# Kernel tuning notes

Hardware: AMD Instinct MI355X
Metric: run time of the kernel (lower is better)

Reference implementation:

```python
import jax, jax.numpy as jnp
import numpy as np

N = 50000      # nodes
E = 800000     # edges
D = 128        # in = out features (required by Euler residual update)
GRID_SIZE = 5
K = 3          # spline order
GRID_LO, GRID_HI = -1.0, 1.0
EPSILON = 0.001
NUM_BASES = GRID_SIZE + K  # 8


def make_grid(in_features):
    # extended uniform grid: [in, grid_size + 2k + 1]
    h = (GRID_HI - GRID_LO) / GRID_SIZE
    g = jnp.arange(-K, GRID_SIZE + K + 1, dtype=jnp.float32) * h + GRID_LO
    return jnp.broadcast_to(g, (in_features, g.shape[0]))


def b_splines(x, grid):
    # x: [N, in]; grid: [in, g+2k+1] -> bases: [N, in, g+k] (Cox-de Boor)
    xe = x[..., None]
    bases = ((xe >= grid[:, :-1]) & (xe < grid[:, 1:])).astype(x.dtype)
    for j in range(1, K + 1):
        left = (xe - grid[:, : -(j + 1)]) / (grid[:, j:-1] - grid[:, : -(j + 1)])
        right = (grid[:, j + 1:] - xe) / (grid[:, j + 1:] - grid[:, 1:-j])
        bases = left * bases[..., :-1] + right * bases[..., 1:]
    return bases


def kan_transform(x, base_w, spline_w, grid):
    # efficient-KAN layer (scale_and_bias=False): silu base branch + spline branch
    base = jax.nn.silu(x) @ base_w.T                    # [N, out]
    sb = b_splines(x, grid)                             # [N, in, g+k]
    spl = jnp.einsum('nib,oib->no', sb, spline_w)       # [N, out]
    return base + spl


def gcn_norm_coeffs(edge_index, n):
    # A_hat symmetric normalization: deg includes self-loop (+1)
    src, dst = edge_index[0], edge_index[1]
    deg = jnp.zeros((n,), jnp.float32).at[dst].add(1.0) + 1.0
    dis = jax.lax.rsqrt(deg)
    return dis[src] * dis[dst]


def setup_inputs() -> dict:
    key = jax.random.key(0)
    ks = jax.random.split(key, 6)
    x = jax.random.uniform(ks[0], (N, D), jnp.float32) * 2.0 - 1.0  # in grid_range
    edge_index = jax.random.randint(ks[1], (2, E), 0, N, dtype=jnp.int64)
    base_w_l = jax.random.normal(ks[2], (D, D), jnp.float32) * (1.0 / np.sqrt(D))
    spline_w_l = jax.random.normal(ks[3], (D, D, NUM_BASES), jnp.float32) * 0.1
    base_w_c = jax.random.normal(ks[4], (D, D), jnp.float32) * (1.0 / np.sqrt(D))
    spline_w_c = jax.random.normal(ks[5], (D, D, NUM_BASES), jnp.float32) * 0.1
    return {"x": x, "edge_index": edge_index, "base_w_l": base_w_l,
            "spline_w_l": spline_w_l, "base_w_c": base_w_c,
            "spline_w_c": spline_w_c, "delta_t": 2}


def reference(x, edge_index, base_w_l, spline_w_l, base_w_c, spline_w_c, delta_t):
    grid = make_grid(D)
    src, dst = edge_index[0], edge_index[1]
    norm = gcn_norm_coeffs(edge_index, N)  # [E]

    def layer(h):
        # KANLayer branch on node features
        h_l = kan_transform(h, base_w_l, spline_w_l, grid)
        # KANConv branch: aggregate_first -> normalized scatter-add, then KAN
        msgs = norm[:, None] * h[src]                              # [E, D]
        agg = jax.ops.segment_sum(msgs, dst, num_segments=N)       # [N, D]
        h_c = kan_transform(agg, base_w_c, spline_w_c, grid)
        return h_l + h_c

    for _ in range(int(delta_t)):   # explicit Euler ODE steps
        x = x + EPSILON * layer(x)
    return x
```

## Files before the change

kernel.cpp:

```cpp
#include <hip/hip_runtime.h>
#include <hip/hip_bf16.h>

#define NNODES 50000
#define NEDGES 800000
#define DF 128
#define KW 1152
#define EPS 0.001f
#define XSS 132
#define NB 196

typedef __bf16 bf16x8 __attribute__((ext_vector_type(8)));
typedef __bf16 bf16x4 __attribute__((ext_vector_type(4)));
typedef float  f32x4  __attribute__((ext_vector_type(4)));
typedef unsigned long ulongx2 __attribute__((ext_vector_type(2)));

__global__ void build_wt(const float* __restrict__ bwl, const float* __restrict__ swl,
                         const float* __restrict__ bwc, const float* __restrict__ swc,
                         __bf16* __restrict__ wtl, __bf16* __restrict__ wtc) {
    int gid = blockIdx.x * 256 + threadIdx.x;
    const float* bw = blockIdx.y ? bwc : bwl;
    const float* sw = blockIdx.y ? swc : swl;
    __bf16*      wt = blockIdx.y ? wtc : wtl;
    int o = gid / KW;
    int k = gid - o * KW;
    float v = (k < 128) ? bw[o * DF + k] : sw[o * 1024 + (k - 128)];
    wt[gid] = (__bf16)v;
}

__global__ void cast_x(const float* __restrict__ x, __bf16* __restrict__ xb) {
    int i = blockIdx.x * 256 + threadIdx.x;
    f32x4 a = ((const f32x4*)x)[2 * i];
    f32x4 b = ((const f32x4*)x)[2 * i + 1];
    bf16x8 o;
    o[0] = (__bf16)a[0]; o[1] = (__bf16)a[1]; o[2] = (__bf16)a[2]; o[3] = (__bf16)a[3];
    o[4] = (__bf16)b[0]; o[5] = (__bf16)b[1]; o[6] = (__bf16)b[2]; o[7] = (__bf16)b[3];
    ((bf16x8*)xb)[i] = o;
}

__global__ void deg_count(const int* __restrict__ ei, int* __restrict__ deg) {
    int e = blockIdx.x * 256 + threadIdx.x;
    if (e >= NEDGES) return;
    atomicAdd(&deg[ei[NEDGES + e]], 1);
}

__global__ void scan_part(const int* __restrict__ deg, int* __restrict__ bsum) {
    __shared__ int red[256];
    int t = threadIdx.x;
    int i = blockIdx.x * 256 + t;
    red[t] = (i < NNODES) ? deg[i] : 0;
    __syncthreads();
    for (int off = 128; off > 0; off >>= 1) {
        if (t < off) red[t] += red[t + off];
        __syncthreads();
    }
    if (t == 0) bsum[blockIdx.x] = red[0];
}

__global__ void scan_bsum(const int* __restrict__ bsum, int* __restrict__ boff) {
    __shared__ int buf[256];
    int t = threadIdx.x;
    int v = (t < NB) ? bsum[t] : 0;
    buf[t] = v;
    __syncthreads();
    for (int off = 1; off < 256; off <<= 1) {
        int x = (t >= off) ? buf[t - off] : 0;
        __syncthreads();
        buf[t] += x;
        __syncthreads();
    }
    if (t <= NB) boff[t] = buf[t] - ((t < NB) ? bsum[t] : 0);
}

__global__ void scan_final(const int* __restrict__ deg, const int* __restrict__ boff,
                           int* __restrict__ rowptr) {
    __shared__ int buf[256];
    int t = threadIdx.x;
    int i = blockIdx.x * 256 + t;
    int v = (i < NNODES) ? deg[i] : 0;
    buf[t] = v;
    __syncthreads();
    for (int off = 1; off < 256; off <<= 1) {
        int x = (t >= off) ? buf[t - off] : 0;
        __syncthreads();
        buf[t] += x;
        __syncthreads();
    }
    if (i < NNODES) rowptr[i] = buf[t] - v + boff[blockIdx.x];
    if (blockIdx.x == 0 && t == 0) rowptr[NNODES] = boff[NB];
}

__global__ void fill_csr(const int* __restrict__ ei, const int* __restrict__ deg,
                         const int* __restrict__ rowptr, int* __restrict__ cnt,
                         int* __restrict__ esrc, float* __restrict__ ew) {
    int e = blockIdx.x * 256 + threadIdx.x;
    if (e >= NEDGES) return;
    int s = ei[e];
    int d = ei[NEDGES + e];
    float w = rsqrtf((float)(deg[s] + 1)) * rsqrtf((float)(deg[d] + 1));
    int p = rowptr[d] + atomicAdd(&cnt[d], 1);
    esrc[p] = s;
    ew[p] = w;
}

__global__ __launch_bounds__(256) void agg_gather(
        const int* __restrict__ rowptr, const int* __restrict__ esrc,
        const float* __restrict__ ew, const __bf16* __restrict__ hb,
        __bf16* __restrict__ aggb) {
    const int tid = blockIdx.x * 256 + threadIdx.x;
    const int n = tid >> 5;
    const int l = tid & 31;
    if (n >= NNODES) return;
    int p  = rowptr[n];
    const int pe = rowptr[n + 1];
    f32x4 acc = {0.0f, 0.0f, 0.0f, 0.0f};
    int   cs0, cs1, cs2, cs3;
    float cw0, cw1, cw2, cw3;
    bool have = (p + 3 < pe);
    if (have) {
        cs0 = esrc[p]; cs1 = esrc[p + 1]; cs2 = esrc[p + 2]; cs3 = esrc[p + 3];
        cw0 = ew[p];   cw1 = ew[p + 1];   cw2 = ew[p + 2];   cw3 = ew[p + 3];
    }
    while (have) {
        int np = p + 4;
        bool nh = (np + 3 < pe);
        int   ns0 = 0, ns1 = 0, ns2 = 0, ns3 = 0;
        float nw0 = 0, nw1 = 0, nw2 = 0, nw3 = 0;
        if (nh) {
            ns0 = esrc[np]; ns1 = esrc[np + 1]; ns2 = esrc[np + 2]; ns3 = esrc[np + 3];
            nw0 = ew[np];   nw1 = ew[np + 1];   nw2 = ew[np + 2];   nw3 = ew[np + 3];
        }
        bf16x4 v0 = *(const bf16x4*)(hb + (size_t)cs0 * DF + l * 4);
        bf16x4 v1 = *(const bf16x4*)(hb + (size_t)cs1 * DF + l * 4);
        bf16x4 v2 = *(const bf16x4*)(hb + (size_t)cs2 * DF + l * 4);
        bf16x4 v3 = *(const bf16x4*)(hb + (size_t)cs3 * DF + l * 4);
#pragma unroll
        for (int j = 0; j < 4; ++j)
            acc[j] += cw0 * (float)v0[j] + cw1 * (float)v1[j]
                    + cw2 * (float)v2[j] + cw3 * (float)v3[j];
        p = np;
        cs0 = ns0; cs1 = ns1; cs2 = ns2; cs3 = ns3;
        cw0 = nw0; cw1 = nw1; cw2 = nw2; cw3 = nw3;
        have = nh;
    }
    for (; p < pe; ++p) {
        int   s0 = esrc[p];
        float w0 = ew[p];
        bf16x4 v0 = *(const bf16x4*)(hb + (size_t)s0 * DF + l * 4);
#pragma unroll
        for (int j = 0; j < 4; ++j) acc[j] += w0 * (float)v0[j];
    }
    bf16x4 o;
#pragma unroll
    for (int j = 0; j < 4; ++j) o[j] = (__bf16)acc[j];
    *(bf16x4*)(aggb + (size_t)n * DF + l * 4) = o;
}

__global__ __launch_bounds__(256, 4) void kan_step(
        const float* __restrict__ h,
        const __bf16* __restrict__ xb,
        const __bf16* __restrict__ aggb,
        const __bf16* __restrict__ wtl, const __bf16* __restrict__ wtc,
        float* __restrict__ out, __bf16* __restrict__ outb) {
    __shared__ __bf16 Bs[2][128 * 40];
    __shared__ __bf16 Xs[64 * XSS];

    const int tid  = threadIdx.x;
    const int lane = tid & 63;
    const int w    = tid >> 6;
    const int q    = lane >> 4, l15 = lane & 15;
    const int n0   = blockIdx.x * 64;

    const int so = tid & 127, sh = tid >> 7;
    const int bbase = so * 40 + sh * 16;
    const size_t wrow = (size_t)so * KW + sh * 16;

    const int xrow = tid >> 2, xseg = tid & 3;
    const bool xok = (n0 + xrow) < NNODES;
    const size_t xgoff = (size_t)(n0 + xrow) * DF + xseg * 32;
    const int xloff = xrow * XSS + xseg * 32;

    const int myrow = w * 16 + l15;

    f32x4 acc[8] = {};
    uint4 g0, g1;

    auto stage_x = [&](const __bf16* src) {
        uint4 v0 = {}, v1 = {}, v2 = {}, v3 = {};
        if (xok) {
            const uint4* g = (const uint4*)(src + xgoff);
            v0 = g[0]; v1 = g[1]; v2 = g[2]; v3 = g[3];
        }
        *(uint4*)&Xs[xloff]      = v0;
        *(uint4*)&Xs[xloff + 8]  = v1;
        *(uint4*)&Xs[xloff + 16] = v2;
        *(uint4*)&Xs[xloff + 24] = v3;
    };

    auto loadB = [&](int tn) {
        const __bf16* wtp = (tn >= 36) ? wtc : wtl;
        const int ck = (tn >= 36) ? tn - 36 : tn;
        const uint4* gp = (const uint4*)(wtp + wrow + ck * 32);
        g0 = gp[0]; g1 = gp[1];
    };
    auto writeB = [&](int buf) {
        *(uint4*)&Bs[buf][bbase]     = g0;
        *(uint4*)&Bs[buf][bbase + 8] = g1;
    };

    auto spline_pack = [&](float x) -> bf16x8 {
        float f  = __builtin_fmaf(x, 2.5f, 5.5f);
        float fi = floorf(f);
        int  idx = (int)fi;
        float u  = f - fi;
        float u2 = u * u, u3 = u2 * u;
        float om = 1.0f - u;
        float Wa = u3 * (1.0f / 6.0f);
        float Wb = (((-3.0f * u + 3.0f) * u + 3.0f) * u + 1.0f) * (1.0f / 6.0f);
        float Wc = ((3.0f * u - 6.0f) * u2 + 4.0f) * (1.0f / 6.0f);
        float Wd = om * om * om * (1.0f / 6.0f);
        unsigned long p =
              (unsigned long)__builtin_bit_cast(unsigned short, (__bf16)Wd)
            | ((unsigned long)__builtin_bit_cast(unsigned short, (__bf16)Wc) << 16)
            | ((unsigned long)__builtin_bit_cast(unsigned short, (__bf16)Wb) << 32)
            | ((unsigned long)__builtin_bit_cast(unsigned short, (__bf16)Wa) << 48);
        int tt = idx - 3;
        unsigned long lo, hi;
        if (tt >= 0) {
            int s = (tt & 3) * 16;
            unsigned long sv = p << s;
            unsigned long cr = (p >> (63 - s)) >> 1;
            bool hh = tt >= 4;
            lo = hh ? 0ul : sv;
            hi = hh ? sv : cr;
            if (tt >= 8) { lo = 0; hi = 0; }
        } else {
            int s = (-tt) * 16;
            lo = (tt >= -3) ? (p >> (s & 63)) : 0ul;
            hi = 0;
        }
        ulongx2 r; r[0] = lo; r[1] = hi;
        return __builtin_bit_cast(bf16x8, r);
    };

    auto silu8 = [&](const __bf16* xs) -> bf16x8 {
        bf16x8 v = *(const bf16x8*)xs;
        bf16x8 o;
#pragma unroll
        for (int j = 0; j < 8; ++j) {
            float x = (float)v[j];
            o[j] = (__bf16)(x / (1.0f + __expf(-x)));
        }
        return o;
    };

    stage_x(xb);
    loadB(0); writeB(0);
    __syncthreads();

#pragma unroll 2
    for (int t = 0; t < 72; ++t) {
        const int buf = t & 1;
        const bool more = t + 1 < 72;
        if (more) loadB(t + 1);

        const int ck = (t >= 36) ? t - 36 : t;
        bf16x8 a;
        if (ck < 4) {
            a = silu8(&Xs[myrow * XSS + ck * 32 + q * 8]);
        } else {
            unsigned short u0 = *(const unsigned short*)&Xs[myrow * XSS + (ck - 4) * 4 + q];
            a = spline_pack(__builtin_bit_cast(float, (unsigned)u0 << 16));
        }

        bf16x8 bF[8];
#pragma unroll
        for (int nj = 0; nj < 8; ++nj)
            bF[nj] = *(const bf16x8*)&Bs[buf][(nj * 16 + l15) * 40 + q * 8];
#pragma unroll
        for (int nj = 0; nj < 8; ++nj)
            acc[nj] = __builtin_amdgcn_mfma_f32_16x16x32_bf16(a, bF[nj], acc[nj], 0, 0, 0);

        if (t == 35) {
            __syncthreads();
            stage_x(aggb);
        }
        if (more) writeB(buf ^ 1);
        __syncthreads();
    }

#pragma unroll
    for (int nj = 0; nj < 8; ++nj) {
#pragma unroll
        for (int r = 0; r < 4; ++r) {
            int row = n0 + w * 16 + q * 4 + r;
            int col = nj * 16 + l15;
            if (row < NNODES) {
                size_t idx = (size_t)row * DF + col;
                float v = h[idx] + EPS * acc[nj][r];
                out[idx]  = v;
                outb[idx] = (__bf16)v;
            }
        }
    }
}

extern "C" void kernel_launch(void* const* d_in, const int* in_sizes, int n_in,
                              void* d_out, int out_size, void* d_ws, size_t ws_size,
                              hipStream_t stream) {
    const float* x   = (const float*)d_in[0];
    const int*   ei  = (const int*)d_in[1];
    const float* bwl = (const float*)d_in[2];
    const float* swl = (const float*)d_in[3];
    const float* bwc = (const float*)d_in[4];
    const float* swc = (const float*)d_in[5];
    float* out = (float*)d_out;

    char* ws = (char*)d_ws;
    int*    deg    = (int*)  (ws + 0);
    int*    cnt    = (int*)  (ws + 200000);
    int*    rowptr = (int*)  (ws + 400000);
    int*    bsum   = (int*)  (ws + 600064);
    int*    boff   = (int*)  (ws + 600896);
    int*    esrc   = (int*)  (ws + 601728);
    float*  ew     = (float*)(ws + 3801728);
    __bf16* xb     = (__bf16*)(ws + 7001728);
    __bf16* aggb   = (__bf16*)(ws + 19801728);
    __bf16* wtl    = (__bf16*)(ws + 32601728);
    __bf16* wtc    = (__bf16*)(ws + 32896640);

    build_wt<<<dim3((DF * KW) / 256, 2), 256, 0, stream>>>(bwl, swl, bwc, swc, wtl, wtc);
    cast_x<<<3125, 256, 0, stream>>>(x, xb);

    hipMemsetAsync(deg, 0, 400000, stream);
    deg_count<<<3125, 256, 0, stream>>>(ei, deg);
    scan_part<<<NB, 256, 0, stream>>>(deg, bsum);
    scan_bsum<<<1, 256, 0, stream>>>(bsum, boff);
    scan_final<<<NB, 256, 0, stream>>>(deg, boff, rowptr);
    fill_csr<<<3125, 256, 0, stream>>>(ei, deg, rowptr, cnt, esrc, ew);

    const int gemm_grid = (NNODES + 63) / 64;
    const float* h = x;
    for (int step = 0; step < 2; ++step) {
        agg_gather<<<6250, 256, 0, stream>>>(rowptr, esrc, ew, xb, aggb);
        kan_step<<<gemm_grid, 256, 0, stream>>>(h, xb, aggb, wtl, wtc, out, xb);
        h = out;
    }
}
```

Measured before the change: 398.8 us.

## Use direct global-to-LDS loads with triple-buffered weights and swizzled X tile

Replaces the register-staged double-buffered weight tile with async global_load_lds into a three-buffer ring, so weight fetches land in LDS without passing through VGPRs and run two steps ahead. Manual vmcnt waits and raw barriers replace __syncthreads. The padded X tile is replaced by an XOR-swizzled layout to avoid bank conflicts. The aggregate features are prefetched into registers up front, and MFMA issue gets raised priority. These changes add register pressure from the prefetched aggregate and depend on fragile hand-written waitcnt and barrier ordering.

After: 388.9 us. 1.03x faster.

```diff
diff --git a/kernel.cpp b/kernel.cpp
--- a/kernel.cpp
+++ b/kernel.cpp
@@ -6,13 +6,16 @@
 #define DF 128
 #define KW 1152
 #define EPS 0.001f
-#define XSS 132
 #define NB 196
 
 typedef __bf16 bf16x8 __attribute__((ext_vector_type(8)));
 typedef __bf16 bf16x4 __attribute__((ext_vector_type(4)));
 typedef float  f32x4  __attribute__((ext_vector_type(4)));
 typedef unsigned long ulongx2 __attribute__((ext_vector_type(2)));
+
+#define GLOAD16(g, l) __builtin_amdgcn_global_load_lds( \
+    (const __attribute__((address_space(1))) unsigned int*)(g), \
+    (__attribute__((address_space(3))) unsigned int*)(l), 16, 0, 0)
 
 __global__ void build_wt(const float* __restrict__ bwl, const float* __restrict__ swl,
                          const float* __restrict__ bwc, const float* __restrict__ swc,
@@ -161,50 +164,41 @@
         const __bf16* __restrict__ aggb,
         const __bf16* __restrict__ wtl, const __bf16* __restrict__ wtc,
         float* __restrict__ out, __bf16* __restrict__ outb) {
-    __shared__ __bf16 Bs[2][128 * 40];
-    __shared__ __bf16 Xs[64 * XSS];
+    __shared__ __bf16 Bs[3][128 * 32];
+    __shared__ __bf16 Xs[64 * 128];
 
     const int tid  = threadIdx.x;
     const int lane = tid & 63;
     const int w    = tid >> 6;
     const int q    = lane >> 4, l15 = lane & 15;
     const int n0   = blockIdx.x * 64;
-
-    const int so = tid & 127, sh = tid >> 7;
-    const int bbase = so * 40 + sh * 16;
-    const size_t wrow = (size_t)so * KW + sh * 16;
+    const int myrow = w * 16 + l15;
+    const int msw   = myrow & 7;
+
+    const int r0 = w * 16 + (lane >> 2);
+    const size_t gb0 = (size_t)r0 * KW + (size_t)(lane & 3) * 8;
+    const size_t gb1 = gb0 + (size_t)64 * KW;
 
     const int xrow = tid >> 2, xseg = tid & 3;
     const bool xok = (n0 + xrow) < NNODES;
     const size_t xgoff = (size_t)(n0 + xrow) * DF + xseg * 32;
-    const int xloff = xrow * XSS + xseg * 32;
-
-    const int myrow = w * 16 + l15;
 
     f32x4 acc[8] = {};
-    uint4 g0, g1;
-
-    auto stage_x = [&](const __bf16* src) {
-        uint4 v0 = {}, v1 = {}, v2 = {}, v3 = {};
-        if (xok) {
-            const uint4* g = (const uint4*)(src + xgoff);
-            v0 = g[0]; v1 = g[1]; v2 = g[2]; v3 = g[3];
-        }
-        *(uint4*)&Xs[xloff]      = v0;
-        *(uint4*)&Xs[xloff + 8]  = v1;
-        *(uint4*)&Xs[xloff + 16] = v2;
-        *(uint4*)&Xs[xloff + 24] = v3;
-    };
-
-    auto loadB = [&](int tn) {
-        const __bf16* wtp = (tn >= 36) ? wtc : wtl;
-        const int ck = (tn >= 36) ? tn - 36 : tn;
-        const uint4* gp = (const uint4*)(wtp + wrow + ck * 32);
-        g0 = gp[0]; g1 = gp[1];
-    };
-    auto writeB = [&](int buf) {
-        *(uint4*)&Bs[buf][bbase]     = g0;
-        *(uint4*)&Bs[buf][bbase + 8] = g1;
+
+    auto xs_write = [&](uint4 v0, uint4 v1, uint4 v2, uint4 v3) {
+        const int gl = xrow * 16 + xseg * 4;
+        const int sw = xrow & 7;
+        *(uint4*)&Xs[(size_t)((gl + 0) ^ sw) * 8] = v0;
+        *(uint4*)&Xs[(size_t)((gl + 1) ^ sw) * 8] = v1;
+        *(uint4*)&Xs[(size_t)((gl + 2) ^ sw) * 8] = v2;
+        *(uint4*)&Xs[(size_t)((gl + 3) ^ sw) * 8] = v3;
+    };
+
+    auto stageB = [&](int t2, int sb) {
+        const __bf16* wtp = (t2 >= 36) ? wtc : wtl;
+        const int k0 = ((t2 >= 36) ? t2 - 36 : t2) * 32;
+        GLOAD16(wtp + gb0 + k0, &Bs[sb][(w * 16) * 32]);
+        GLOAD16(wtp + gb1 + k0, &Bs[sb][(64 + w * 16) * 32]);
     };
 
     auto spline_pack = [&](float x) -> bf16x8 {
@@ -253,40 +247,68 @@
         return o;
     };
 
-    stage_x(xb);
-    loadB(0); writeB(0);
-    __syncthreads();
-
-#pragma unroll 2
-    for (int t = 0; t < 72; ++t) {
-        const int buf = t & 1;
-        const bool more = t + 1 < 72;
-        if (more) loadB(t + 1);
+    uint4 a0 = {}, a1 = {}, a2 = {}, a3 = {};
+    uint4 c0 = {}, c1 = {}, c2 = {}, c3 = {};
+    if (xok) {
+        const uint4* ga = (const uint4*)(xb + xgoff);
+        a0 = ga[0]; a1 = ga[1]; a2 = ga[2]; a3 = ga[3];
+        const uint4* gc = (const uint4*)(aggb + xgoff);
+        c0 = gc[0]; c1 = gc[1]; c2 = gc[2]; c3 = gc[3];
+    }
+    xs_write(a0, a1, a2, a3);
+    stageB(0, 0);
+    stageB(1, 1);
+    asm volatile("s_waitcnt lgkmcnt(0)" ::: "memory");
+
+    auto body = [&](int t, int cb, int sb, bool doStage, bool last) {
+        if (last) asm volatile("s_waitcnt vmcnt(0)" ::: "memory");
+        else      asm volatile("s_waitcnt vmcnt(2)" ::: "memory");
+        __builtin_amdgcn_s_barrier();
+        __builtin_amdgcn_sched_barrier(0);
+
+        if (t == 36) {
+            xs_write(c0, c1, c2, c3);
+            asm volatile("s_waitcnt lgkmcnt(0)" ::: "memory");
+            __builtin_amdgcn_s_barrier();
+            __builtin_amdgcn_sched_barrier(0);
+        }
+
+        if (doStage) stageB(t + 2, sb);
 
         const int ck = (t >= 36) ? t - 36 : t;
         bf16x8 a;
         if (ck < 4) {
-            a = silu8(&Xs[myrow * XSS + ck * 32 + q * 8]);
+            const int g = (myrow * 16 + ck * 4 + q) ^ msw;
+            a = silu8(&Xs[(size_t)g * 8]);
         } else {
-            unsigned short u0 = *(const unsigned short*)&Xs[myrow * XSS + (ck - 4) * 4 + q];
+            const int f = (ck - 4) * 4 + q;
+            const int g = (myrow * 16 + (f >> 3)) ^ msw;
+            unsigned short u0 =
+                *(const unsigned short*)&Xs[(size_t)g * 8 + (f & 7)];
             a = spline_pack(__builtin_bit_cast(float, (unsigned)u0 << 16));
         }
 
         bf16x8 bF[8];
 #pragma unroll
         for (int nj = 0; nj < 8; ++nj)
-            bF[nj] = *(const bf16x8*)&Bs[buf][(nj * 16 + l15) * 40 + q * 8];
+            bF[nj] = *(const bf16x8*)&Bs[cb][(nj * 16 + l15) * 32 + q * 8];
+        __builtin_amdgcn_s_setprio(1);
 #pragma unroll
         for (int nj = 0; nj < 8; ++nj)
             acc[nj] = __builtin_amdgcn_mfma_f32_16x16x32_bf16(a, bF[nj], acc[nj], 0, 0, 0);
-
-        if (t == 35) {
-            __syncthreads();
-            stage_x(aggb);
-        }
-        if (more) writeB(buf ^ 1);
-        __syncthreads();
-    }
+        __builtin_amdgcn_s_setprio(0);
+    };
+
+    int cb = 0, sb = 2;
+#pragma unroll 3
+    for (int t = 0; t < 69; ++t) {
+        body(t, cb, sb, true, false);
+        cb = (cb == 2) ? 0 : cb + 1;
+        sb = (sb == 2) ? 0 : sb + 1;
+    }
+    body(69, 0, 2, true,  false);
+    body(70, 1, 0, false, false);
+    body(71, 2, 0, false, true);
 
 #pragma unroll
     for (int nj = 0; nj < 8; ++nj) {
```
